# Kernel optimization log

Measured on AMD Instinct MI355X. Metric: run time of the kernel, lower is better.

The kernel has to match this reference:

```python
import jax, jax.numpy as jnp
import numpy as np


def setup_inputs() -> dict:
    key = jax.random.key(0)
    ks = jax.random.split(key, 6)
    B_, S, D_in, D_out, R, E = 4, 2048, 2048, 2048, 64, 16
    x = jax.random.normal(ks[0], (B_, S, D_in), dtype=jnp.float32)
    W_base = jax.random.normal(ks[1], (D_out, D_in), dtype=jnp.float32) * (D_in ** -0.5)
    b_base = jax.random.normal(ks[2], (D_out,), dtype=jnp.float32) * 0.02
    # orthogonal rows, as get_orthogonal_matrix(reservoir_size, in_features)
    G = np.asarray(jax.random.normal(ks[3], (D_in, R), dtype=jnp.float32))
    Q, _ = np.linalg.qr(G)  # [D_in, R] orthonormal columns
    A = jnp.asarray(Q.T, dtype=jnp.float32)  # [R, D_in]
    # B initialized to zeros in the module; use small random so delta is nontrivial
    Bmat = jax.random.normal(ks[4], (E, D_out, R), dtype=jnp.float32) * 0.02
    W_router = jax.random.normal(ks[5], (E, D_in), dtype=jnp.float32) * 0.02
    return {"x": x, "W_base": W_base, "b_base": b_base, "A": A, "B": Bmat,
            "W_router": W_router, "top_k": 2}


def reference(x, W_base, b_base, A, B, W_router, top_k):
    E = W_router.shape[0]
    base_output = jnp.einsum('bsi,oi->bso', x, W_base) + b_base          # [B,S,D_out]
    res_hidden = jnp.einsum('bsi,ri->bsr', x, A)                          # [B,S,R]
    router_logits = jnp.einsum('bsi,ei->bse', x, W_router)                # [B,S,E]
    routing_weights = jax.nn.softmax(router_logits, axis=-1)
    if top_k > 0 and top_k < E:
        _, top_idx = jax.lax.top_k(routing_weights, top_k)                # [B,S,k]
        mask = jax.nn.one_hot(top_idx, E, dtype=routing_weights.dtype).sum(axis=-2)
        routing_weights = routing_weights * mask
        routing_weights = routing_weights / (routing_weights.sum(axis=-1, keepdims=True) + 1e-6)
    # contract experts+rank without materializing [B,S,E,D_out]
    h = jnp.einsum('bsr,bse->bser', res_hidden, routing_weights)          # [B,S,E,R] (small)
    delta = jnp.einsum('bser,edr->bsd', h, B)                             # [B,S,D_out]
    return base_output + delta
```

## Files before the change

kernel.cpp:

```cpp
#include <hip/hip_runtime.h>
#include <hip/hip_bf16.h>

#define D_IN  2048
#define D_OUT 2048
#define RNK   64
#define NE    16
#define KTOT  3072

typedef __attribute__((ext_vector_type(8))) short bf16x8;
typedef __attribute__((ext_vector_type(4))) float f32x4;

__device__ __forceinline__ void async_ld16(const void* g, void* l) {
    __builtin_amdgcn_global_load_lds(
        (const __attribute__((address_space(1))) void*)g,
        (__attribute__((address_space(3))) void*)l,
        16, 0, 0);
}

__global__ __launch_bounds__(384) void castwa_kernel(
    const float* __restrict__ Wb, const float* __restrict__ Bm,
    const float* __restrict__ A,
    __hip_bfloat16* __restrict__ Wc, __hip_bfloat16* __restrict__ Ab)
{
    const int c = threadIdx.x * 8;
    const float* src;
    __hip_bfloat16* dst;
    if (blockIdx.x < D_OUT) {
        const int n = blockIdx.x;
        if (c < D_IN) {
            src = Wb + (size_t)n * D_IN + c;
        } else {
            const int j = c - D_IN;
            const int e = j >> 6, r = j & 63;
            src = Bm + ((size_t)e * D_OUT + n) * RNK + r;
        }
        dst = Wc + (size_t)n * KTOT + c;
    } else {
        if (c >= D_IN) return;
        const int r = blockIdx.x - D_OUT;
        src = A + (size_t)r * D_IN + c;
        dst = Ab + (size_t)r * D_IN + c;
    }
    const float4 a = *(const float4*)src;
    const float4 b = *(const float4*)(src + 4);
    const float vv[8] = {a.x, a.y, a.z, a.w, b.x, b.y, b.z, b.w};
    union { bf16x8 v; __hip_bfloat16 h[8]; } u;
#pragma unroll
    for (int q = 0; q < 8; ++q) u.h[q] = __float2bfloat16(vv[q]);
    *(bf16x8*)dst = u.v;
}

__global__ __launch_bounds__(512) void prep2_kernel(
    const float* __restrict__ x, const float* __restrict__ Wr,
    const __hip_bfloat16* __restrict__ Ab,
    const int* __restrict__ topk_p, __hip_bfloat16* __restrict__ Xc)
{
    __shared__ __align__(16) char smem[81920];
    __hip_bfloat16* xb = (__hip_bfloat16*)smem;
    float* stage = (float*)(smem + 65536);
    float* red = (float*)smem;
    float* wf  = (float*)(smem + 65536);

    const int tid = threadIdx.x;
    const int wave = tid >> 6, lane = tid & 63;
    const int qm = lane & 15, quad = lane >> 4;
    const int t0 = blockIdx.x * 16;
    const int tA = t0 + wave * 2;

    float acc[NE][2];
#pragma unroll
    for (int e = 0; e < NE; ++e) { acc[e][0] = 0.f; acc[e][1] = 0.f; }

    const float4* x4 = (const float4*)x;
    float4 xv[2], xn[2];
    xv[0] = x4[(size_t)tA * 512 + lane];
    xv[1] = x4[(size_t)(tA + 1) * 512 + lane];

    for (int c = 0; c < 8; ++c) {
        async_ld16(Wr + (size_t)wave * D_IN + c * 256 + lane * 4,
                   (void*)(stage + wave * 256));
        async_ld16(Wr + (size_t)(wave + 8) * D_IN + c * 256 + lane * 4,
                   (void*)(stage + (wave + 8) * 256));
        if (c < 7) {
            xn[0] = x4[(size_t)tA * 512 + (c + 1) * 64 + lane];
            xn[1] = x4[(size_t)(tA + 1) * 512 + (c + 1) * 64 + lane];
        }
        __syncthreads();

#pragma unroll
        for (int t = 0; t < 2; ++t) {
            const int tl = wave * 2 + t;
            union { short4 v; __hip_bfloat16 h[4]; } u;
            u.h[0] = __float2bfloat16(xv[t].x); u.h[1] = __float2bfloat16(xv[t].y);
            u.h[2] = __float2bfloat16(xv[t].z); u.h[3] = __float2bfloat16(xv[t].w);
            *(short4*)(Xc + (size_t)(t0 + tl) * KTOT + c * 256 + lane * 4) = u.v;
            const int gg = c * 32 + (lane >> 1);
            const int pg = gg ^ (tl & 7);
            *(short4*)((char*)xb + tl * 4096 + pg * 16 + (lane & 1) * 8) = u.v;
        }
        const float4* wr4 = (const float4*)stage;
#pragma unroll
        for (int e = 0; e < NE; ++e) {
            const float4 wv = wr4[e * 64 + lane];
            acc[e][0] += xv[0].x*wv.x + xv[0].y*wv.y + xv[0].z*wv.z + xv[0].w*wv.w;
            acc[e][1] += xv[1].x*wv.x + xv[1].y*wv.y + xv[1].z*wv.z + xv[1].w*wv.w;
        }
        __syncthreads();
        if (c < 7) { xv[0] = xn[0]; xv[1] = xn[1]; }
    }

#pragma unroll
    for (int off = 32; off; off >>= 1)
#pragma unroll
        for (int e = 0; e < NE; ++e) {
            acc[e][0] += __shfl_xor(acc[e][0], off, 64);
            acc[e][1] += __shfl_xor(acc[e][1], off, 64);
        }
    if (lane < 2) {
        const int tt = lane;
        const int k = topk_p[0];
        float m = -1e30f;
#pragma unroll
        for (int e = 0; e < NE; ++e) m = fmaxf(m, acc[e][tt]);
        float w[NE]; float ssum = 0.f;
#pragma unroll
        for (int e = 0; e < NE; ++e) { w[e] = __expf(acc[e][tt] - m); ssum += w[e]; }
        const float inv = 1.f / ssum;
#pragma unroll
        for (int e = 0; e < NE; ++e) w[e] *= inv;
        float* wfout = wf + (size_t)(wave * 2 + tt) * NE;
        if (k > 0 && k < NE) {
            int chosen[NE];
#pragma unroll
            for (int e = 0; e < NE; ++e) chosen[e] = 0;
            float ksum = 0.f;
            for (int it = 0; it < k; ++it) {
                int bi = 0; float bv = -1.f;
                for (int e = 0; e < NE; ++e)
                    if (!chosen[e] && w[e] > bv) { bv = w[e]; bi = e; }
                chosen[bi] = 1; ksum += bv;
            }
            const float rinv = 1.f / (ksum + 1e-6f);
            for (int e = 0; e < NE; ++e) wfout[e] = chosen[e] ? w[e] * rinv : 0.f;
        } else {
            for (int e = 0; e < NE; ++e) wfout[e] = w[e];
        }
    }

    f32x4 racc[4] = {};
    const int kb = wave * 256;
#pragma unroll
    for (int s = 0; s < 4; ++s) {
        const int k0 = kb + s * 64;
        const int gg0 = (k0 >> 3) + quad;
        const bf16x8 a0 = *(const bf16x8*)((char*)xb + qm * 4096 + ((gg0 ^ (qm & 7)) * 16));
        const bf16x8 a1 = *(const bf16x8*)((char*)xb + qm * 4096 + (((gg0 + 4) ^ (qm & 7)) * 16));
        bf16x8 b0[4], b1[4];
#pragma unroll
        for (int nf = 0; nf < 4; ++nf) {
            const __hip_bfloat16* bp = Ab + (size_t)(qm + nf * 16) * D_IN + k0 + quad * 8;
            b0[nf] = *(const bf16x8*)bp;
            b1[nf] = *(const bf16x8*)(bp + 32);
        }
#pragma unroll
        for (int nf = 0; nf < 4; ++nf) {
            racc[nf] = __builtin_amdgcn_mfma_f32_16x16x32_bf16(a0, b0[nf], racc[nf], 0, 0, 0);
            racc[nf] = __builtin_amdgcn_mfma_f32_16x16x32_bf16(a1, b1[nf], racc[nf], 0, 0, 0);
        }
    }
    __syncthreads();

#pragma unroll
    for (int nf = 0; nf < 4; ++nf)
#pragma unroll
        for (int r = 0; r < 4; ++r)
            red[(wave * 16 + quad * 4 + r) * 64 + nf * 16 + qm] = racc[nf][r];
    __syncthreads();

#pragma unroll
    for (int it = 0; it < 4; ++it) {
        const int s = it * 512 + tid;
        const int t = s >> 7;
        const int chunk = s & 127;
        const int e = chunk >> 3, r0 = (chunk & 7) * 8;
        const float wgt = wf[t * 16 + e];
        float4 s0 = {0.f, 0.f, 0.f, 0.f}, s1 = {0.f, 0.f, 0.f, 0.f};
#pragma unroll
        for (int w2 = 0; w2 < 8; ++w2) {
            const float4 p0 = ((const float4*)red)[(w2 * 16 + t) * 16 + (r0 >> 2)];
            const float4 p1 = ((const float4*)red)[(w2 * 16 + t) * 16 + (r0 >> 2) + 1];
            s0.x += p0.x; s0.y += p0.y; s0.z += p0.z; s0.w += p0.w;
            s1.x += p1.x; s1.y += p1.y; s1.z += p1.z; s1.w += p1.w;
        }
        union { bf16x8 v; __hip_bfloat16 h[8]; } u;
        u.h[0] = __float2bfloat16(wgt * s0.x); u.h[1] = __float2bfloat16(wgt * s0.y);
        u.h[2] = __float2bfloat16(wgt * s0.z); u.h[3] = __float2bfloat16(wgt * s0.w);
        u.h[4] = __float2bfloat16(wgt * s1.x); u.h[5] = __float2bfloat16(wgt * s1.y);
        u.h[6] = __float2bfloat16(wgt * s1.z); u.h[7] = __float2bfloat16(wgt * s1.w);
        *(bf16x8*)(Xc + (size_t)(t0 + t) * KTOT + D_IN + chunk * 8) = u.v;
    }
}

__global__ __launch_bounds__(256) void gemm_kernel(
    const __hip_bfloat16* __restrict__ Am,
    const __hip_bfloat16* __restrict__ Bm,
    const float* __restrict__ bias,
    float* __restrict__ C, int M, int N)
{
    __shared__ __hip_bfloat16 lds_a[128 * 64];
    __shared__ __hip_bfloat16 lds_b[128 * 64];
    const int tid = threadIdx.x;
    const int wave = tid >> 6, lane = tid & 63;
    const int bm = blockIdx.x, bn = blockIdx.y;
    const int qm = lane & 15, quad = lane >> 4;
    const int ar = lane >> 3;
    const int ac = ((lane & 7) ^ ar) * 8;

    f32x4 acc[4][4] = {};
    const int wm = (wave >> 1) * 64, wn = (wave & 1) * 64;

    const __hip_bfloat16* ga[4];
    const __hip_bfloat16* gb[4];
#pragma unroll
    for (int j = 0; j < 4; ++j) {
        ga[j] = Am + (size_t)(bm * 128 + wave * 32 + j * 8 + ar) * KTOT + ac;
        gb[j] = Bm + (size_t)(bn * 128 + wave * 32 + j * 8 + ar) * KTOT + ac;
    }

    for (int k0 = 0; k0 < KTOT; k0 += 64) {
#pragma unroll
        for (int j = 0; j < 4; ++j) {
            async_ld16(ga[j], (void*)&lds_a[(wave * 4 + j) * 512]);
            async_ld16(gb[j], (void*)&lds_b[(wave * 4 + j) * 512]);
            ga[j] += 64; gb[j] += 64;
        }
        __syncthreads();

#pragma unroll
        for (int kk = 0; kk < 64; kk += 32) {
            const int cg = (kk >> 3) + quad;
            const int sw = (cg ^ (qm & 7)) * 8;
            bf16x8 af[4], bfr[4];
#pragma unroll
            for (int i = 0; i < 4; ++i)
                af[i] = *(const bf16x8*)&lds_a[(wm + i * 16 + qm) * 64 + sw];
#pragma unroll
            for (int j = 0; j < 4; ++j)
                bfr[j] = *(const bf16x8*)&lds_b[(wn + j * 16 + qm) * 64 + sw];
#pragma unroll
            for (int i = 0; i < 4; ++i)
#pragma unroll
                for (int j = 0; j < 4; ++j)
                    acc[i][j] = __builtin_amdgcn_mfma_f32_16x16x32_bf16(
                        af[i], bfr[j], acc[i][j], 0, 0, 0);
        }
        __syncthreads();
    }

    const size_t row0 = (size_t)bm * 128 + wm;
    const int col0 = bn * 128 + wn;
#pragma unroll
    for (int j = 0; j < 4; ++j) {
        const int col = col0 + j * 16 + qm;
        const float bb = bias[col];
#pragma unroll
        for (int i = 0; i < 4; ++i) {
#pragma unroll
            for (int r = 0; r < 4; ++r) {
                const size_t row = row0 + i * 16 + quad * 4 + r;
                C[row * (size_t)N + col] = acc[i][j][r] + bb;
            }
        }
    }
}

extern "C" void kernel_launch(void* const* d_in, const int* in_sizes, int n_in,
                              void* d_out, int out_size, void* d_ws, size_t ws_size,
                              hipStream_t stream) {
    const float* x    = (const float*)d_in[0];
    const float* Wb   = (const float*)d_in[1];
    const float* bb   = (const float*)d_in[2];
    const float* A    = (const float*)d_in[3];
    const float* Bm   = (const float*)d_in[4];
    const float* Wr   = (const float*)d_in[5];
    const int*   topk = (const int*)d_in[6];
    float* out = (float*)d_out;
    const int T = in_sizes[0] / D_IN;

    __hip_bfloat16* Xc = (__hip_bfloat16*)d_ws;
    __hip_bfloat16* Wc = (__hip_bfloat16*)((char*)d_ws + (size_t)T * KTOT * 2);
    __hip_bfloat16* Ab = (__hip_bfloat16*)d_out;

    castwa_kernel<<<D_OUT + RNK, 384, 0, stream>>>(Wb, Bm, A, Wc, Ab);
    prep2_kernel<<<T / 16, 512, 0, stream>>>(x, Wr, Ab, topk, Xc);
    gemm_kernel<<<dim3(T / 128, D_OUT / 128), 256, 0, stream>>>(Xc, Wc, bb, out, T, D_OUT);
}
```

Before: 278.5 us.

## Replace GEMM with 256x256-tile double-buffered pipelined kernel

Swaps the 128x128 single-buffered GEMM for a 512-thread kernel that computes 256x256 tiles with 64-deep K slices. LDS is double-buffered (128KB) and global-to-LDS loads for the next K tile are overlapped with MFMA work through explicit waitcnt, barriers and setprio phases. Blocks are remapped so neighbouring blocks share operand rows, for better L2 reuse. The aim is to hide load latency and cut global traffic per FLOP. In exchange the grid shrinks to 256 blocks, there are hard-coded sizes (T=8192 assumed), and more registers are used.

Result: no change. 277.7 us (-0.3%).

```diff
diff --git a/kernel.cpp b/kernel.cpp
--- a/kernel.cpp
+++ b/kernel.cpp
@@ -6,6 +6,7 @@
 #define RNK   64
 #define NE    16
 #define KTOT  3072
+#define NTILE 48
 
 typedef __attribute__((ext_vector_type(8))) short bf16x8;
 typedef __attribute__((ext_vector_type(4))) float f32x4;
@@ -201,74 +202,115 @@
     }
 }
 
-__global__ __launch_bounds__(256) void gemm_kernel(
+#define LDA(BO, MH, i, kk) (*(const bf16x8*)(ldsc + (BO) + \
+    ((MH) * 128 + wm2 * 64 + (i) * 16 + qm) * 128 + \
+    ((((kk) * 4 + quad) ^ (qm & 7)) * 16)))
+#define LDB(BO, NH, j, kk) (*(const bf16x8*)(ldsc + 65536 + (BO) + \
+    ((NH) * 128 + wn4 * 32 + (j) * 16 + qm) * 128 + \
+    ((((kk) * 4 + quad) ^ (qm & 7)) * 16)))
+
+#define PHASE(BO, MH, NH, STAGE_STMT, WAIT_STMT) do { \
+    bf16x8 af0[4], bv0[2], af1[4], bv1[2]; \
+    _Pragma("unroll") for (int i = 0; i < 4; ++i) af0[i] = LDA(BO, MH, i, 0); \
+    _Pragma("unroll") for (int j = 0; j < 2; ++j) bv0[j] = LDB(BO, NH, j, 0); \
+    STAGE_STMT; \
+    WAIT_STMT; \
+    __builtin_amdgcn_sched_barrier(0); \
+    __builtin_amdgcn_s_barrier(); \
+    __builtin_amdgcn_sched_barrier(0); \
+    __builtin_amdgcn_s_setprio(1); \
+    _Pragma("unroll") for (int i = 0; i < 4; ++i) \
+    _Pragma("unroll") for (int j = 0; j < 2; ++j) \
+        acc[(MH)*4+i][(NH)*2+j] = __builtin_amdgcn_mfma_f32_16x16x32_bf16( \
+            af0[i], bv0[j], acc[(MH)*4+i][(NH)*2+j], 0, 0, 0); \
+    _Pragma("unroll") for (int i = 0; i < 4; ++i) af1[i] = LDA(BO, MH, i, 1); \
+    _Pragma("unroll") for (int j = 0; j < 2; ++j) bv1[j] = LDB(BO, NH, j, 1); \
+    _Pragma("unroll") for (int i = 0; i < 4; ++i) \
+    _Pragma("unroll") for (int j = 0; j < 2; ++j) \
+        acc[(MH)*4+i][(NH)*2+j] = __builtin_amdgcn_mfma_f32_16x16x32_bf16( \
+            af1[i], bv1[j], acc[(MH)*4+i][(NH)*2+j], 0, 0, 0); \
+    __builtin_amdgcn_s_setprio(0); \
+    __builtin_amdgcn_sched_barrier(0); \
+    __builtin_amdgcn_s_barrier(); \
+    __builtin_amdgcn_sched_barrier(0); \
+} while (0)
+
+__global__ __launch_bounds__(512, 2) void gemm2_kernel(
     const __hip_bfloat16* __restrict__ Am,
     const __hip_bfloat16* __restrict__ Bm,
     const float* __restrict__ bias,
-    float* __restrict__ C, int M, int N)
+    float* __restrict__ C)
 {
-    __shared__ __hip_bfloat16 lds_a[128 * 64];
-    __shared__ __hip_bfloat16 lds_b[128 * 64];
+    __shared__ __align__(16) char smem[131072];
+    char* ldsc = smem;
     const int tid = threadIdx.x;
-    const int wave = tid >> 6, lane = tid & 63;
-    const int bm = blockIdx.x, bn = blockIdx.y;
+    const int w = tid >> 6, lane = tid & 63;
     const int qm = lane & 15, quad = lane >> 4;
-    const int ar = lane >> 3;
-    const int ac = ((lane & 7) ^ ar) * 8;
-
-    f32x4 acc[4][4] = {};
-    const int wm = (wave >> 1) * 64, wn = (wave & 1) * 64;
-
-    const __hip_bfloat16* ga[4];
-    const __hip_bfloat16* gb[4];
-#pragma unroll
-    for (int j = 0; j < 4; ++j) {
-        ga[j] = Am + (size_t)(bm * 128 + wave * 32 + j * 8 + ar) * KTOT + ac;
-        gb[j] = Bm + (size_t)(bn * 128 + wave * 32 + j * 8 + ar) * KTOT + ac;
-    }
-
-    for (int k0 = 0; k0 < KTOT; k0 += 64) {
-#pragma unroll
-        for (int j = 0; j < 4; ++j) {
-            async_ld16(ga[j], (void*)&lds_a[(wave * 4 + j) * 512]);
-            async_ld16(gb[j], (void*)&lds_b[(wave * 4 + j) * 512]);
-            ga[j] += 64; gb[j] += 64;
-        }
-        __syncthreads();
-
-#pragma unroll
-        for (int kk = 0; kk < 64; kk += 32) {
-            const int cg = (kk >> 3) + quad;
-            const int sw = (cg ^ (qm & 7)) * 8;
-            bf16x8 af[4], bfr[4];
-#pragma unroll
-            for (int i = 0; i < 4; ++i)
-                af[i] = *(const bf16x8*)&lds_a[(wm + i * 16 + qm) * 64 + sw];
-#pragma unroll
-            for (int j = 0; j < 4; ++j)
-                bfr[j] = *(const bf16x8*)&lds_b[(wn + j * 16 + qm) * 64 + sw];
-#pragma unroll
-            for (int i = 0; i < 4; ++i)
-#pragma unroll
-                for (int j = 0; j < 4; ++j)
-                    acc[i][j] = __builtin_amdgcn_mfma_f32_16x16x32_bf16(
-                        af[i], bfr[j], acc[i][j], 0, 0, 0);
-        }
-        __syncthreads();
-    }
-
-    const size_t row0 = (size_t)bm * 128 + wm;
-    const int col0 = bn * 128 + wn;
-#pragma unroll
-    for (int j = 0; j < 4; ++j) {
-        const int col = col0 + j * 16 + qm;
+    const int wm2 = w >> 2, wn4 = w & 3;
+
+    int flat = blockIdx.y * gridDim.x + blockIdx.x;
+    flat = (flat & 7) * 32 + (flat >> 3);
+    const int bm = flat & 31, bn = flat >> 5;
+
+    const int rb0 = w * 16 + (lane >> 3);
+    const int rb1 = rb0 + 8;
+    const int gs0 = (lane & 7) ^ (rb0 & 7);
+    const int gs1 = (lane & 7) ^ (rb1 & 7);
+    const __hip_bfloat16* pA0 = Am + (size_t)(bm * 256 + rb0) * KTOT + gs0 * 8;
+    const __hip_bfloat16* pA1 = Am + (size_t)(bm * 256 + rb1) * KTOT + gs1 * 8;
+    const __hip_bfloat16* pB0 = Bm + (size_t)(bn * 256 + rb0) * KTOT + gs0 * 8;
+    const __hip_bfloat16* pB1 = Bm + (size_t)(bn * 256 + rb1) * KTOT + gs1 * 8;
+
+    f32x4 acc[8][4] = {};
+
+    auto stage_pair = [&](int tn, int hh) {
+        const size_t ko = (size_t)tn * 64;
+        const size_t ho = (size_t)hh * (128 * KTOT);
+        char* da = ldsc + (tn & 1) * 32768 + hh * 16384 + w * 2048;
+        async_ld16(pA0 + ho + ko, da);
+        async_ld16(pA1 + ho + ko, da + 1024);
+        char* db = ldsc + 65536 + (tn & 1) * 32768 + hh * 16384 + w * 2048;
+        async_ld16(pB0 + ho + ko, db);
+        async_ld16(pB1 + ho + ko, db + 1024);
+    };
+
+    stage_pair(0, 0); stage_pair(0, 1);
+    asm volatile("s_waitcnt vmcnt(0)" ::: "memory");
+    __builtin_amdgcn_s_barrier();
+
+    for (int t = 0; t < NTILE - 1; ++t) {
+        const int bo = (t & 1) * 32768;
+        PHASE(bo, 0, 0, stage_pair(t + 1, 0),
+              asm volatile("s_waitcnt vmcnt(4)" ::: "memory"));
+        PHASE(bo, 1, 0, stage_pair(t + 1, 1), );
+        PHASE(bo, 0, 1, , );
+        PHASE(bo, 1, 1, ,
+              asm volatile("s_waitcnt vmcnt(4)" ::: "memory"));
+    }
+    {
+        const int bo = 32768;
+        PHASE(bo, 0, 0, , asm volatile("s_waitcnt vmcnt(0)" ::: "memory"));
+        PHASE(bo, 1, 0, , );
+        PHASE(bo, 0, 1, , );
+        PHASE(bo, 1, 1, , );
+    }
+
+    const size_t row0 = (size_t)bm * 256;
+    const int col0 = bn * 256;
+#pragma unroll
+    for (int nh = 0; nh < 2; ++nh)
+#pragma unroll
+    for (int j = 0; j < 2; ++j) {
+        const int col = col0 + nh * 128 + wn4 * 32 + j * 16 + qm;
         const float bb = bias[col];
 #pragma unroll
+        for (int mh = 0; mh < 2; ++mh)
+#pragma unroll
         for (int i = 0; i < 4; ++i) {
 #pragma unroll
             for (int r = 0; r < 4; ++r) {
-                const size_t row = row0 + i * 16 + quad * 4 + r;
-                C[row * (size_t)N + col] = acc[i][j][r] + bb;
+                const size_t row = row0 + mh * 128 + wm2 * 64 + i * 16 + quad * 4 + r;
+                C[row * D_OUT + col] = acc[mh * 4 + i][nh * 2 + j][r] + bb;
             }
         }
     }
@@ -293,5 +335,5 @@
 
     castwa_kernel<<<D_OUT + RNK, 384, 0, stream>>>(Wb, Bm, A, Wc, Ab);
     prep2_kernel<<<T / 16, 512, 0, stream>>>(x, Wr, Ab, topk, Xc);
-    gemm_kernel<<<dim3(T / 128, D_OUT / 128), 256, 0, stream>>>(Xc, Wc, bb, out, T, D_OUT);
-}
+    gemm2_kernel<<<dim3(32, 8), 512, 0, stream>>>(Xc, Wc, bb, out);
+}
```
